# Kernel optimization log

Hardware: AMD Instinct MI355X
Metric: run time of the kernel (lower is better)

## Reference

```python
import jax, jax.numpy as jnp
import numpy as np

H = 512

def setup_inputs() -> dict:
    key = jax.random.key(0)
    ks = jax.random.split(key, 8)
    s = 1.0 / np.sqrt(H)
    return {
        "encoder_outputs": jax.random.normal(ks[0], (64, 2048, H), dtype=jnp.float32),
        "decoder_hidden": jax.random.normal(ks[1], (64, H), dtype=jnp.float32),
        "W1": jax.random.uniform(ks[2], (H, H), jnp.float32, -s, s),
        "b1": jax.random.uniform(ks[3], (H,), jnp.float32, -s, s),
        "W2": jax.random.uniform(ks[4], (H, H), jnp.float32, -s, s),
        "b2": jax.random.uniform(ks[5], (H,), jnp.float32, -s, s),
        "V": jax.random.uniform(ks[6], (H,), jnp.float32, -s, s),  # V weight (1, H) squeezed
        "bv": jax.random.uniform(ks[7], (1,), jnp.float32, -s, s),
    }

def reference(encoder_outputs, decoder_hidden, W1, b1, W2, b2, V, bv):
    # proj of encoder outputs: [B,S,H]; proj of decoder hidden: [B,1,H]
    enc_proj = jnp.einsum('bsh,oh->bso', encoder_outputs, W1) + b1
    dec_proj = (jnp.einsum('bh,oh->bo', decoder_hidden, W2) + b2)[:, None, :]
    energy = jnp.tanh(enc_proj + dec_proj)                      # [B,S,H]
    scores = jnp.einsum('bsh,h->bs', energy, V) + bv[0]          # [B,S]
    attn = jax.nn.softmax(scores, axis=1)                        # [B,S]
    context = jnp.einsum('bs,bsh->bh', attn, encoder_outputs)    # [B,H]
    return context, attn
```

## Files before the change

kernel.cpp:

```cpp
#include <hip/hip_runtime.h>
#include <hip/hip_bf16.h>

typedef __attribute__((ext_vector_type(4))) float f32x4;
typedef __attribute__((ext_vector_type(8))) short s16x8;
typedef __attribute__((ext_vector_type(4))) unsigned short u16x4;
typedef __attribute__((ext_vector_type(8))) __bf16 bf16x8;

#define HDIM 512
#define SEQ  2048
#define NB   64
#define BM   64
#define NBLK ((NB * SEQ) / BM)
#define CPB  (SEQ / BM)

static __device__ __forceinline__ unsigned short f2bf(float f) {
  unsigned u = __float_as_uint(f);
  u += 0x7fffu + ((u >> 16) & 1u);
  return (unsigned short)(u >> 16);
}
static __device__ __forceinline__ float bf2f(unsigned short v) {
  return __uint_as_float(((unsigned)v) << 16);
}

static __device__ __forceinline__ f32x4 mfma16(s16x8 a, s16x8 b, f32x4 c) {
  return __builtin_amdgcn_mfma_f32_16x16x32_bf16(
      __builtin_bit_cast(bf16x8, a), __builtin_bit_cast(bf16x8, b), c, 0, 0, 0);
}

#define BLOADG(dst, sp)                                                        \
  do {                                                                         \
    asm volatile("global_load_dwordx4 %0, %1, %2 offset:0"                     \
                 : "=&v"((dst)[0]) : "v"(voff), "s"(sp));                      \
    asm volatile("global_load_dwordx4 %0, %1, %2 offset:1024"                  \
                 : "=&v"((dst)[1]) : "v"(voff), "s"(sp));                      \
    asm volatile("global_load_dwordx4 %0, %1, %2 offset:2048"                  \
                 : "=&v"((dst)[2]) : "v"(voff), "s"(sp));                      \
    asm volatile("global_load_dwordx4 %0, %1, %2 offset:3072"                  \
                 : "=&v"((dst)[3]) : "v"(voff), "s"(sp));                      \
  } while (0)

#define SLOAD(dst, s)                                                          \
  asm volatile("global_load_dwordx4 %0, %1, %2"                                \
               : "=&v"(dst) : "v"(aoff), "s"(encblk + (s) * 32))

#define WAITV(N)                                                               \
  do {                                                                         \
    asm volatile("s_waitcnt vmcnt(%0)" :: "i"(N) : "memory");                  \
    __builtin_amdgcn_sched_barrier(0);                                         \
  } while (0)

#define PACKW(src, s)                                                          \
  do {                                                                         \
    u16x4 pk;                                                                  \
    pk.x = f2bf((src).x); pk.y = f2bf((src).y);                                \
    pk.z = f2bf((src).z); pk.w = f2bf((src).w);                                \
    *(u16x4*)((char*)Asm + wrow * 1024 +                                       \
              (((((s) * 4) + (wc >> 1)) ^ wr7) * 16) + (wc & 1) * 8) = pk;     \
  } while (0)

__global__ void prep(const float* __restrict__ w1, unsigned short* __restrict__ o,
                     const float* __restrict__ dec, const float* __restrict__ W2,
                     const float* __restrict__ b1, const float* __restrict__ b2,
                     float* __restrict__ zfull) {
  const int bx = blockIdx.x, tid = threadIdx.x;
  if (bx < 128) {
    int id = bx * 256 + tid;
    int kk = id >> 11, n = (id >> 2) & 511, r4 = id & 3;
    const float* src = w1 + (long)n * HDIM + kk * 32 + r4 * 8;
    f32x4 v0 = *(const f32x4*)src;
    f32x4 v1 = *(const f32x4*)(src + 4);
    u16x4 a, b;
    a.x = f2bf(v0.x); a.y = f2bf(v0.y); a.z = f2bf(v0.z); a.w = f2bf(v0.w);
    b.x = f2bf(v1.x); b.y = f2bf(v1.y); b.z = f2bf(v1.z); b.w = f2bf(v1.w);
    unsigned short* dst = o + (long)id * 8;
    *(u16x4*)dst = a;
    *(u16x4*)(dst + 4) = b;
  } else {
    const int idx = bx - 128;
    const int b = idx >> 1, oc = idx & 1;
    const int oo = oc * 256 + tid;
    __shared__ float d_s[HDIM];
    d_s[tid] = dec[b * HDIM + tid];
    d_s[tid + 256] = dec[b * HDIM + tid + 256];
    __syncthreads();
    const float* w = W2 + (long)oo * HDIM;
    float s = 0.f;
#pragma unroll 4
    for (int k = 0; k < HDIM; k += 4) {
      f32x4 v = *(const f32x4*)(w + k);
      s += v.x * d_s[k] + v.y * d_s[k + 1] + v.z * d_s[k + 2] + v.w * d_s[k + 3];
    }
    zfull[b * HDIM + oo] = s + b1[oo] + b2[oo];
  }
}

__global__ __launch_bounds__(512, 4)
void gemm_fused(const float* __restrict__ enc, const unsigned short* __restrict__ w1k,
                const float* __restrict__ zfull, const float* __restrict__ V,
                const float* __restrict__ bv, float* __restrict__ scores,
                unsigned short* __restrict__ pctx, float* __restrict__ ml) {
  __shared__ __align__(16) char pool[67840];
  unsigned short* Asm = (unsigned short*)pool;
  float* red  = (float*)(pool + 65536);
  float* plds = (float*)(pool + 67584);
  float* pcr  = (float*)pool;

  const int tid = threadIdx.x;
  const int wid = tid >> 6;
  const int lane = tid & 63;
  const long m0 = (long)blockIdx.x * BM;
  const int b = (int)(m0 >> 11);

  const int r4 = lane >> 4, c15 = lane & 15, c7 = c15 & 7;
  const char* Ab = (const char*)Asm;
  const unsigned voff = (unsigned)((wid * 64 + c15) * 64 + r4 * 16);
  const int widu = __builtin_amdgcn_readfirstlane(wid);

  const int wrow = tid >> 3, wc = tid & 7, wr7 = wrow & 7;
  const float* encblk = enc + m0 * HDIM;
  const unsigned aoff = (unsigned)(wrow * 2048 + wc * 16);

  {
    f32x4 pa, pb, pc, pd, pe, pf, pg, ph;
    SLOAD(pa, 0); SLOAD(pb, 1); SLOAD(pc, 2); SLOAD(pd, 3);
    SLOAD(pe, 4); SLOAD(pf, 5); SLOAD(pg, 6); SLOAD(ph, 7);
    WAITV(4);
    PACKW(pa, 0); PACKW(pb, 1); PACKW(pc, 2); PACKW(pd, 3);
    SLOAD(pa, 8); SLOAD(pb, 9); SLOAD(pc, 10); SLOAD(pd, 11);
    WAITV(4);
    PACKW(pe, 4); PACKW(pf, 5); PACKW(pg, 6); PACKW(ph, 7);
    SLOAD(pe, 12); SLOAD(pf, 13); SLOAD(pg, 14); SLOAD(ph, 15);
    WAITV(4);
    PACKW(pa, 8); PACKW(pb, 9); PACKW(pc, 10); PACKW(pd, 11);
    WAITV(0);
    PACKW(pe, 12); PACKW(pf, 13); PACKW(pg, 14); PACKW(ph, 15);
  }
  __syncthreads();

  f32x4 acc[4][4] = {};
  s16x8 bX[4], bY[4];

  BLOADG(bX, w1k + ((widu & 15) * 16384));

#pragma unroll
  for (int kk = 0; kk < 16; ++kk) {
    const int ke = (kk + widu) & 15;
    s16x8* cur = (kk & 1) ? bY : bX;
    s16x8* nxt = (kk & 1) ? bX : bY;

    s16x8 af[4];
    const int abase = c15 * 1024 + (((ke * 4 + r4) ^ c7) * 16);
#pragma unroll
    for (int mf = 0; mf < 4; ++mf)
      af[mf] = *(const s16x8*)(Ab + abase + mf * 16384);

    if (kk < 15)
      BLOADG(nxt, w1k + ((((kk + 1) + widu) & 15) * 16384));

    __builtin_amdgcn_s_setprio(1);
    if (kk < 15) {
      WAITV(7);
#pragma unroll
      for (int mf = 0; mf < 4; ++mf) acc[mf][0] = mfma16(af[mf], cur[0], acc[mf][0]);
      WAITV(6);
#pragma unroll
      for (int mf = 0; mf < 4; ++mf) acc[mf][1] = mfma16(af[mf], cur[1], acc[mf][1]);
      WAITV(5);
#pragma unroll
      for (int mf = 0; mf < 4; ++mf) acc[mf][2] = mfma16(af[mf], cur[2], acc[mf][2]);
      WAITV(4);
#pragma unroll
      for (int mf = 0; mf < 4; ++mf) acc[mf][3] = mfma16(af[mf], cur[3], acc[mf][3]);
    } else {
      WAITV(3);
#pragma unroll
      for (int mf = 0; mf < 4; ++mf) acc[mf][0] = mfma16(af[mf], cur[0], acc[mf][0]);
      WAITV(2);
#pragma unroll
      for (int mf = 0; mf < 4; ++mf) acc[mf][1] = mfma16(af[mf], cur[1], acc[mf][1]);
      WAITV(1);
#pragma unroll
      for (int mf = 0; mf < 4; ++mf) acc[mf][2] = mfma16(af[mf], cur[2], acc[mf][2]);
      WAITV(0);
#pragma unroll
      for (int mf = 0; mf < 4; ++mf) acc[mf][3] = mfma16(af[mf], cur[3], acc[mf][3]);
    }
    __builtin_amdgcn_s_setprio(0);
  }

  float zr[4], vr[4];
#pragma unroll
  for (int nf = 0; nf < 4; ++nf) {
    const int n = wid * 64 + nf * 16 + c15;
    zr[nf] = zfull[b * HDIM + n];
    vr[nf] = V[n];
  }
#pragma unroll
  for (int mf = 0; mf < 4; ++mf) {
#pragma unroll
    for (int j = 0; j < 4; ++j) {
      float s = 0.f;
#pragma unroll
      for (int nf = 0; nf < 4; ++nf) {
        float x = acc[mf][nf][j] + zr[nf];
        float e = __expf(2.f * x);
        float t = 1.f - 2.f * __builtin_amdgcn_rcpf(e + 1.f);
        s += t * vr[nf];
      }
      s += __shfl_xor(s, 1); s += __shfl_xor(s, 2);
      s += __shfl_xor(s, 4); s += __shfl_xor(s, 8);
      if (c15 == 0) red[wid * BM + mf * 16 + r4 * 4 + j] = s;
    }
  }
  __syncthreads();

  if (tid < BM) {
    float s = 0.f;
#pragma unroll
    for (int w = 0; w < 8; ++w) s += red[w * BM + tid];
    s += bv[0];
    scores[m0 + tid] = s;
    float mc = s;
#pragma unroll
    for (int off = 1; off < 64; off <<= 1) mc = fmaxf(mc, __shfl_xor(mc, off));
    float p = __expf(s - mc);
    plds[tid] = p;
    float lc = p;
#pragma unroll
    for (int off = 1; off < 64; off <<= 1) lc += __shfl_xor(lc, off);
    if (tid == 0) { ml[blockIdx.x * 2] = mc; ml[blockIdx.x * 2 + 1] = lc; }
  }
  __syncthreads();

  float c8[8] = {};
#pragma unroll
  for (int rr = 0; rr < 8; ++rr) {
    const int r = wid * 8 + rr;
    s16x8 v = *(const s16x8*)(Ab + r * 1024 + ((lane ^ rr) * 16));
    const float p = plds[r];
#pragma unroll
    for (int e = 0; e < 8; ++e)
      c8[e] += p * bf2f((unsigned short)v[e]);
  }
  __syncthreads();
  {
    f32x4 w0, w1;
    w0.x = c8[0]; w0.y = c8[1]; w0.z = c8[2]; w0.w = c8[3];
    w1.x = c8[4]; w1.y = c8[5]; w1.z = c8[6]; w1.w = c8[7];
    *(f32x4*)((char*)pcr + wid * 2048 + lane * 32) = w0;
    *(f32x4*)((char*)pcr + wid * 2048 + lane * 32 + 16) = w1;
  }
  __syncthreads();
  {
    float s = 0.f;
#pragma unroll
    for (int g = 0; g < 8; ++g) s += pcr[g * 512 + tid];
    pctx[(long)blockIdx.x * HDIM + tid] = f2bf(s);
  }
}

__global__ void combine(float* __restrict__ attn, const unsigned short* __restrict__ pctx,
                        const float* __restrict__ ml, float* __restrict__ ctx) {
  const int b = blockIdx.x, tid = threadIdx.x;
  const int lane = tid & 63;
  float m = -1e30f, l = 0.f;
  if (lane < CPB) {
    m = ml[(b * CPB + lane) * 2];
    l = ml[(b * CPB + lane) * 2 + 1];
  }
  float M = m;
#pragma unroll
  for (int off = 1; off < 64; off <<= 1) M = fmaxf(M, __shfl_xor(M, off));
  float le = (lane < CPB) ? l * __expf(m - M) : 0.f;
  float L = le;
#pragma unroll
  for (int off = 1; off < 64; off <<= 1) L += __shfl_xor(L, off);
  const float invL = 1.f / L;

  __shared__ float wc[CPB];
  if (tid < CPB) wc[tid] = __expf(ml[(b * CPB + tid) * 2] - M) * invL;

  float sv[4];
#pragma unroll
  for (int i = 0; i < 4; ++i) sv[i] = attn[(long)b * SEQ + i * 512 + tid];
#pragma unroll
  for (int i = 0; i < 4; ++i)
    attn[(long)b * SEQ + i * 512 + tid] = __expf(sv[i] - M) * invL;

  __syncthreads();
  float a = 0.f;
#pragma unroll 8
  for (int c = 0; c < CPB; ++c)
    a += bf2f(pctx[(long)(b * CPB + c) * HDIM + tid]) * wc[c];
  ctx[(long)b * HDIM + tid] = a;
}

extern "C" void kernel_launch(void* const* d_in, const int* in_sizes, int n_in,
                              void* d_out, int out_size, void* d_ws, size_t ws_size,
                              hipStream_t stream) {
  const float* enc = (const float*)d_in[0];
  const float* dec = (const float*)d_in[1];
  const float* W1  = (const float*)d_in[2];
  const float* b1  = (const float*)d_in[3];
  const float* W2  = (const float*)d_in[4];
  const float* b2  = (const float*)d_in[5];
  const float* V   = (const float*)d_in[6];
  const float* bv  = (const float*)d_in[7];

  float* out  = (float*)d_out;
  float* ctx  = out;
  float* attn = out + NB * HDIM;

  char* ws = (char*)d_ws;
  unsigned short* w1k  = (unsigned short*)ws;
  float*          zful = (float*)(ws + 524288);
  unsigned short* pctx = (unsigned short*)(ws + 655360);
  float*          mlb  = (float*)(ws + 2752512);
  (void)in_sizes; (void)n_in; (void)out_size; (void)ws_size;

  prep<<<256, 256, 0, stream>>>(W1, w1k, dec, W2, b1, b2, zful);
  gemm_fused<<<NBLK, 512, 0, stream>>>(enc, w1k, zful, V, bv, attn, pctx, mlb);
  combine<<<NB, 512, 0, stream>>>(attn, pctx, mlb, ctx);
}
```

Before: 118.1 us.

## Double GEMM row tile to 128 rows per block to reuse W1 fragments

Raises the row tile from 64 to 128 sequence positions per block. Each wave now runs 8 M-fragments against every loaded W1 slice, halving W1 global reads per output row, and LDS grows to about 135KB. The softmax partial reduction becomes a cross-wave reduction through LDS, and occupancy drops from 4 to 2 blocks per CU. The larger accumulator array raises register pressure, and the smaller grid may leave CUs less busy.

```diff
diff --git a/kernel.cpp b/kernel.cpp
--- a/kernel.cpp
+++ b/kernel.cpp
@@ -9,7 +9,7 @@
 #define HDIM 512
 #define SEQ  2048
 #define NB   64
-#define BM   64
+#define BM   128
 #define NBLK ((NB * SEQ) / BM)
 #define CPB  (SEQ / BM)
 
@@ -42,6 +42,9 @@
 #define SLOAD(dst, s)                                                          \
   asm volatile("global_load_dwordx4 %0, %1, %2"                                \
                : "=&v"(dst) : "v"(aoff), "s"(encblk + (s) * 32))
+#define SLOAD2(dst, s)                                                         \
+  asm volatile("global_load_dwordx4 %0, %1, %2"                                \
+               : "=&v"(dst) : "v"(aoff), "s"(encblk + 32768 + (s) * 32))
 
 #define WAITV(N)                                                               \
   do {                                                                         \
@@ -49,12 +52,12 @@
     __builtin_amdgcn_sched_barrier(0);                                         \
   } while (0)
 
-#define PACKW(src, s)                                                          \
+#define PACKWR(src, s, rv)                                                     \
   do {                                                                         \
     u16x4 pk;                                                                  \
     pk.x = f2bf((src).x); pk.y = f2bf((src).y);                                \
     pk.z = f2bf((src).z); pk.w = f2bf((src).w);                                \
-    *(u16x4*)((char*)Asm + wrow * 1024 +                                       \
+    *(u16x4*)((char*)Asm + (rv) * 1024 +                                       \
               (((((s) * 4) + (wc >> 1)) ^ wr7) * 16) + (wc & 1) * 8) = pk;     \
   } while (0)
 
@@ -94,15 +97,17 @@
   }
 }
 
-__global__ __launch_bounds__(512, 4)
+__global__ __launch_bounds__(512, 2)
 void gemm_fused(const float* __restrict__ enc, const unsigned short* __restrict__ w1k,
                 const float* __restrict__ zfull, const float* __restrict__ V,
                 const float* __restrict__ bv, float* __restrict__ scores,
                 unsigned short* __restrict__ pctx, float* __restrict__ ml) {
-  __shared__ __align__(16) char pool[67840];
+  __shared__ __align__(16) char pool[135744];
   unsigned short* Asm = (unsigned short*)pool;
-  float* red  = (float*)(pool + 65536);
-  float* plds = (float*)(pool + 67584);
+  float* red  = (float*)(pool + 131072);
+  float* plds = (float*)(pool + 135168);
+  float* mred = (float*)(pool + 135680);
+  float* lred = (float*)(pool + 135712);
   float* pcr  = (float*)pool;
 
   const int tid = threadIdx.x;
@@ -121,23 +126,40 @@
   const unsigned aoff = (unsigned)(wrow * 2048 + wc * 16);
 
   {
-    f32x4 pa, pb, pc, pd, pe, pf, pg, ph;
-    SLOAD(pa, 0); SLOAD(pb, 1); SLOAD(pc, 2); SLOAD(pd, 3);
-    SLOAD(pe, 4); SLOAD(pf, 5); SLOAD(pg, 6); SLOAD(ph, 7);
-    WAITV(4);
-    PACKW(pa, 0); PACKW(pb, 1); PACKW(pc, 2); PACKW(pd, 3);
-    SLOAD(pa, 8); SLOAD(pb, 9); SLOAD(pc, 10); SLOAD(pd, 11);
-    WAITV(4);
-    PACKW(pe, 4); PACKW(pf, 5); PACKW(pg, 6); PACKW(ph, 7);
-    SLOAD(pe, 12); SLOAD(pf, 13); SLOAD(pg, 14); SLOAD(ph, 15);
-    WAITV(4);
-    PACKW(pa, 8); PACKW(pb, 9); PACKW(pc, 10); PACKW(pd, 11);
+    f32x4 p0, p1, p2, p3, p4, p5, p6, p7;
+    f32x4 q0, q1, q2, q3, q4, q5, q6, q7;
+    SLOAD(p0, 0); SLOAD2(p1, 0); SLOAD(p2, 1); SLOAD2(p3, 1);
+    SLOAD(p4, 2); SLOAD2(p5, 2); SLOAD(p6, 3); SLOAD2(p7, 3);
+    SLOAD(q0, 4); SLOAD2(q1, 4); SLOAD(q2, 5); SLOAD2(q3, 5);
+    SLOAD(q4, 6); SLOAD2(q5, 6); SLOAD(q6, 7); SLOAD2(q7, 7);
+    WAITV(8);
+    PACKWR(p0, 0, wrow); PACKWR(p1, 0, wrow + 64);
+    PACKWR(p2, 1, wrow); PACKWR(p3, 1, wrow + 64);
+    PACKWR(p4, 2, wrow); PACKWR(p5, 2, wrow + 64);
+    PACKWR(p6, 3, wrow); PACKWR(p7, 3, wrow + 64);
+    SLOAD(p0, 8); SLOAD2(p1, 8); SLOAD(p2, 9); SLOAD2(p3, 9);
+    SLOAD(p4, 10); SLOAD2(p5, 10); SLOAD(p6, 11); SLOAD2(p7, 11);
+    WAITV(8);
+    PACKWR(q0, 4, wrow); PACKWR(q1, 4, wrow + 64);
+    PACKWR(q2, 5, wrow); PACKWR(q3, 5, wrow + 64);
+    PACKWR(q4, 6, wrow); PACKWR(q5, 6, wrow + 64);
+    PACKWR(q6, 7, wrow); PACKWR(q7, 7, wrow + 64);
+    SLOAD(q0, 12); SLOAD2(q1, 12); SLOAD(q2, 13); SLOAD2(q3, 13);
+    SLOAD(q4, 14); SLOAD2(q5, 14); SLOAD(q6, 15); SLOAD2(q7, 15);
+    WAITV(8);
+    PACKWR(p0, 8, wrow); PACKWR(p1, 8, wrow + 64);
+    PACKWR(p2, 9, wrow); PACKWR(p3, 9, wrow + 64);
+    PACKWR(p4, 10, wrow); PACKWR(p5, 10, wrow + 64);
+    PACKWR(p6, 11, wrow); PACKWR(p7, 11, wrow + 64);
     WAITV(0);
-    PACKW(pe, 12); PACKW(pf, 13); PACKW(pg, 14); PACKW(ph, 15);
-  }
-  __syncthreads();
-
-  f32x4 acc[4][4] = {};
+    PACKWR(q0, 12, wrow); PACKWR(q1, 12, wrow + 64);
+    PACKWR(q2, 13, wrow); PACKWR(q3, 13, wrow + 64);
+    PACKWR(q4, 14, wrow); PACKWR(q5, 14, wrow + 64);
+    PACKWR(q6, 15, wrow); PACKWR(q7, 15, wrow + 64);
+  }
+  __syncthreads();
+
+  f32x4 acc[8][4] = {};
   s16x8 bX[4], bY[4];
 
   BLOADG(bX, w1k + ((widu & 15) * 16384));
@@ -148,10 +170,10 @@
     s16x8* cur = (kk & 1) ? bY : bX;
     s16x8* nxt = (kk & 1) ? bX : bY;
 
-    s16x8 af[4];
+    s16x8 af[8];
     const int abase = c15 * 1024 + (((ke * 4 + r4) ^ c7) * 16);
 #pragma unroll
-    for (int mf = 0; mf < 4; ++mf)
+    for (int mf = 0; mf < 8; ++mf)
       af[mf] = *(const s16x8*)(Ab + abase + mf * 16384);
 
     if (kk < 15)
@@ -161,29 +183,29 @@
     if (kk < 15) {
       WAITV(7);
 #pragma unroll
-      for (int mf = 0; mf < 4; ++mf) acc[mf][0] = mfma16(af[mf], cur[0], acc[mf][0]);
+      for (int mf = 0; mf < 8; ++mf) acc[mf][0] = mfma16(af[mf], cur[0], acc[mf][0]);
       WAITV(6);
 #pragma unroll
-      for (int mf = 0; mf < 4; ++mf) acc[mf][1] = mfma16(af[mf], cur[1], acc[mf][1]);
+      for (int mf = 0; mf < 8; ++mf) acc[mf][1] = mfma16(af[mf], cur[1], acc[mf][1]);
       WAITV(5);
 #pragma unroll
-      for (int mf = 0; mf < 4; ++mf) acc[mf][2] = mfma16(af[mf], cur[2], acc[mf][2]);
+      for (int mf = 0; mf < 8; ++mf) acc[mf][2] = mfma16(af[mf], cur[2], acc[mf][2]);
       WAITV(4);
 #pragma unroll
-      for (int mf = 0; mf < 4; ++mf) acc[mf][3] = mfma16(af[mf], cur[3], acc[mf][3]);
+      for (int mf = 0; mf < 8; ++mf) acc[mf][3] = mfma16(af[mf], cur[3], acc[mf][3]);
     } else {
       WAITV(3);
 #pragma unroll
-      for (int mf = 0; mf < 4; ++mf) acc[mf][0] = mfma16(af[mf], cur[0], acc[mf][0]);
+      for (int mf = 0; mf < 8; ++mf) acc[mf][0] = mfma16(af[mf], cur[0], acc[mf][0]);
       WAITV(2);
 #pragma unroll
-      for (int mf = 0; mf < 4; ++mf) acc[mf][1] = mfma16(af[mf], cur[1], acc[mf][1]);
+      for (int mf = 0; mf < 8; ++mf) acc[mf][1] = mfma16(af[mf], cur[1], acc[mf][1]);
       WAITV(1);
 #pragma unroll
-      for (int mf = 0; mf < 4; ++mf) acc[mf][2] = mfma16(af[mf], cur[2], acc[mf][2]);
+      for (int mf = 0; mf < 8; ++mf) acc[mf][2] = mfma16(af[mf], cur[2], acc[mf][2]);
       WAITV(0);
 #pragma unroll
-      for (int mf = 0; mf < 4; ++mf) acc[mf][3] = mfma16(af[mf], cur[3], acc[mf][3]);
+      for (int mf = 0; mf < 8; ++mf) acc[mf][3] = mfma16(af[mf], cur[3], acc[mf][3]);
     }
     __builtin_amdgcn_s_setprio(0);
   }
@@ -196,7 +218,7 @@
     vr[nf] = V[n];
   }
 #pragma unroll
-  for (int mf = 0; mf < 4; ++mf) {
+  for (int mf = 0; mf < 8; ++mf) {
 #pragma unroll
     for (int j = 0; j < 4; ++j) {
       float s = 0.f;
@@ -214,29 +236,41 @@
   }
   __syncthreads();
 
+  float sv = 0.f, pv = 0.f;
   if (tid < BM) {
     float s = 0.f;
 #pragma unroll
     for (int w = 0; w < 8; ++w) s += red[w * BM + tid];
     s += bv[0];
     scores[m0 + tid] = s;
-    float mc = s;
-#pragma unroll
-    for (int off = 1; off < 64; off <<= 1) mc = fmaxf(mc, __shfl_xor(mc, off));
-    float p = __expf(s - mc);
-    plds[tid] = p;
-    float lc = p;
-#pragma unroll
-    for (int off = 1; off < 64; off <<= 1) lc += __shfl_xor(lc, off);
-    if (tid == 0) { ml[blockIdx.x * 2] = mc; ml[blockIdx.x * 2 + 1] = lc; }
-  }
-  __syncthreads();
+    sv = s;
+  }
+  float mc = (tid < BM) ? sv : -1e30f;
+#pragma unroll
+  for (int off = 1; off < 64; off <<= 1) mc = fmaxf(mc, __shfl_xor(mc, off));
+  if (lane == 0) mred[wid] = mc;
+  __syncthreads();
+  float M = mred[0];
+#pragma unroll
+  for (int w = 1; w < 8; ++w) M = fmaxf(M, mred[w]);
+  if (tid < BM) { pv = __expf(sv - M); plds[tid] = pv; }
+  float lc = pv;
+#pragma unroll
+  for (int off = 1; off < 64; off <<= 1) lc += __shfl_xor(lc, off);
+  if (lane == 0) lred[wid] = lc;
+  __syncthreads();
+  if (tid == 0) {
+    float L = 0.f;
+#pragma unroll
+    for (int w = 0; w < 8; ++w) L += lred[w];
+    ml[blockIdx.x * 2] = M; ml[blockIdx.x * 2 + 1] = L;
+  }
 
   float c8[8] = {};
 #pragma unroll
-  for (int rr = 0; rr < 8; ++rr) {
-    const int r = wid * 8 + rr;
-    s16x8 v = *(const s16x8*)(Ab + r * 1024 + ((lane ^ rr) * 16));
+  for (int rr = 0; rr < 16; ++rr) {
+    const int r = wid * 16 + rr;
+    s16x8 v = *(const s16x8*)(Ab + r * 1024 + ((lane ^ (rr & 7)) * 16));
     const float p = plds[r];
 #pragma unroll
     for (int e = 0; e < 8; ++e)
```

New measurement: 138.2 us. 1.17x slower.

## Double row tile to 128 with 1024-thread blocks and triple-buffered W1 loads

Applied to the files above, without the earlier changes.

Doubles the encoder rows handled per block to 128 and uses 16 waves, each covering 32 output columns over 8 M-fragments. This raises reuse of each streamed W1 fragment and halves the number of partial-context and max/sum records that combine has to merge. W1 fragments are now triple-buffered with a single wait per k-step, and the per-wave staggered k order is dropped. The block softmax statistics become a cross-wave reduction through LDS. The cost is about 137 KB of LDS per block, which limits each CU to one resident block and reduces latency hiding.

```diff
diff --git a/kernel.cpp b/kernel.cpp
--- a/kernel.cpp
+++ b/kernel.cpp
@@ -9,7 +9,7 @@
 #define HDIM 512
 #define SEQ  2048
 #define NB   64
-#define BM   64
+#define BM   128
 #define NBLK ((NB * SEQ) / BM)
 #define CPB  (SEQ / BM)
 
@@ -27,16 +27,12 @@
       __builtin_bit_cast(bf16x8, a), __builtin_bit_cast(bf16x8, b), c, 0, 0, 0);
 }
 
-#define BLOADG(dst, sp)                                                        \
+#define BLOADG2(dst, sp)                                                       \
   do {                                                                         \
     asm volatile("global_load_dwordx4 %0, %1, %2 offset:0"                     \
                  : "=&v"((dst)[0]) : "v"(voff), "s"(sp));                      \
     asm volatile("global_load_dwordx4 %0, %1, %2 offset:1024"                  \
                  : "=&v"((dst)[1]) : "v"(voff), "s"(sp));                      \
-    asm volatile("global_load_dwordx4 %0, %1, %2 offset:2048"                  \
-                 : "=&v"((dst)[2]) : "v"(voff), "s"(sp));                      \
-    asm volatile("global_load_dwordx4 %0, %1, %2 offset:3072"                  \
-                 : "=&v"((dst)[3]) : "v"(voff), "s"(sp));                      \
   } while (0)
 
 #define SLOAD(dst, s)                                                          \
@@ -94,15 +90,17 @@
   }
 }
 
-__global__ __launch_bounds__(512, 4)
+__global__ __launch_bounds__(1024, 4)
 void gemm_fused(const float* __restrict__ enc, const unsigned short* __restrict__ w1k,
                 const float* __restrict__ zfull, const float* __restrict__ V,
                 const float* __restrict__ bv, float* __restrict__ scores,
                 unsigned short* __restrict__ pctx, float* __restrict__ ml) {
-  __shared__ __align__(16) char pool[67840];
+  __shared__ __align__(16) char pool[139904];
   unsigned short* Asm = (unsigned short*)pool;
-  float* red  = (float*)(pool + 65536);
-  float* plds = (float*)(pool + 67584);
+  float* red  = (float*)(pool + 131072);
+  float* plds = (float*)(pool + 139264);
+  float* mred = (float*)(pool + 139776);
+  float* lred = (float*)(pool + 139840);
   float* pcr  = (float*)pool;
 
   const int tid = threadIdx.x;
@@ -113,8 +111,7 @@
 
   const int r4 = lane >> 4, c15 = lane & 15, c7 = c15 & 7;
   const char* Ab = (const char*)Asm;
-  const unsigned voff = (unsigned)((wid * 64 + c15) * 64 + r4 * 16);
-  const int widu = __builtin_amdgcn_readfirstlane(wid);
+  const unsigned voff = (unsigned)((wid * 32 + c15) * 64 + r4 * 16);
 
   const int wrow = tid >> 3, wc = tid & 7, wr7 = wrow & 7;
   const float* encblk = enc + m0 * HDIM;
@@ -137,71 +134,47 @@
   }
   __syncthreads();
 
-  f32x4 acc[4][4] = {};
-  s16x8 bX[4], bY[4];
-
-  BLOADG(bX, w1k + ((widu & 15) * 16384));
+  f32x4 acc[8][2] = {};
+  s16x8 bq[3][2];
+
+  BLOADG2(bq[0], w1k);
+  BLOADG2(bq[1], w1k + 16384);
 
 #pragma unroll
   for (int kk = 0; kk < 16; ++kk) {
-    const int ke = (kk + widu) & 15;
-    s16x8* cur = (kk & 1) ? bY : bX;
-    s16x8* nxt = (kk & 1) ? bX : bY;
-
-    s16x8 af[4];
-    const int abase = c15 * 1024 + (((ke * 4 + r4) ^ c7) * 16);
-#pragma unroll
-    for (int mf = 0; mf < 4; ++mf)
-      af[mf] = *(const s16x8*)(Ab + abase + mf * 16384);
-
-    if (kk < 15)
-      BLOADG(nxt, w1k + ((((kk + 1) + widu) & 15) * 16384));
-
+    if (kk < 14)
+      BLOADG2(bq[(kk + 2) % 3], w1k + (kk + 2) * 16384);
+
+    if (kk < 14)      WAITV(4);
+    else if (kk == 14) WAITV(2);
+    else               WAITV(0);
+
+    const int abase = c15 * 1024 + (((kk * 4 + r4) ^ c7) * 16);
+    const s16x8* cur = bq[kk % 3];
     __builtin_amdgcn_s_setprio(1);
-    if (kk < 15) {
-      WAITV(7);
-#pragma unroll
-      for (int mf = 0; mf < 4; ++mf) acc[mf][0] = mfma16(af[mf], cur[0], acc[mf][0]);
-      WAITV(6);
-#pragma unroll
-      for (int mf = 0; mf < 4; ++mf) acc[mf][1] = mfma16(af[mf], cur[1], acc[mf][1]);
-      WAITV(5);
-#pragma unroll
-      for (int mf = 0; mf < 4; ++mf) acc[mf][2] = mfma16(af[mf], cur[2], acc[mf][2]);
-      WAITV(4);
-#pragma unroll
-      for (int mf = 0; mf < 4; ++mf) acc[mf][3] = mfma16(af[mf], cur[3], acc[mf][3]);
-    } else {
-      WAITV(3);
-#pragma unroll
-      for (int mf = 0; mf < 4; ++mf) acc[mf][0] = mfma16(af[mf], cur[0], acc[mf][0]);
-      WAITV(2);
-#pragma unroll
-      for (int mf = 0; mf < 4; ++mf) acc[mf][1] = mfma16(af[mf], cur[1], acc[mf][1]);
-      WAITV(1);
-#pragma unroll
-      for (int mf = 0; mf < 4; ++mf) acc[mf][2] = mfma16(af[mf], cur[2], acc[mf][2]);
-      WAITV(0);
-#pragma unroll
-      for (int mf = 0; mf < 4; ++mf) acc[mf][3] = mfma16(af[mf], cur[3], acc[mf][3]);
+#pragma unroll
+    for (int mf = 0; mf < 8; ++mf) {
+      s16x8 af = *(const s16x8*)(Ab + abase + mf * 16384);
+      acc[mf][0] = mfma16(af, cur[0], acc[mf][0]);
+      acc[mf][1] = mfma16(af, cur[1], acc[mf][1]);
     }
     __builtin_amdgcn_s_setprio(0);
   }
 
-  float zr[4], vr[4];
-#pragma unroll
-  for (int nf = 0; nf < 4; ++nf) {
-    const int n = wid * 64 + nf * 16 + c15;
+  float zr[2], vr[2];
+#pragma unroll
+  for (int nf = 0; nf < 2; ++nf) {
+    const int n = wid * 32 + nf * 16 + c15;
     zr[nf] = zfull[b * HDIM + n];
     vr[nf] = V[n];
   }
 #pragma unroll
-  for (int mf = 0; mf < 4; ++mf) {
+  for (int mf = 0; mf < 8; ++mf) {
 #pragma unroll
     for (int j = 0; j < 4; ++j) {
       float s = 0.f;
 #pragma unroll
-      for (int nf = 0; nf < 4; ++nf) {
+      for (int nf = 0; nf < 2; ++nf) {
         float x = acc[mf][nf][j] + zr[nf];
         float e = __expf(2.f * x);
         float t = 1.f - 2.f * __builtin_amdgcn_rcpf(e + 1.f);
@@ -214,29 +187,41 @@
   }
   __syncthreads();
 
+  float sv = -1e30f, pv = 0.f;
   if (tid < BM) {
     float s = 0.f;
 #pragma unroll
-    for (int w = 0; w < 8; ++w) s += red[w * BM + tid];
+    for (int w = 0; w < 16; ++w) s += red[w * BM + tid];
     s += bv[0];
     scores[m0 + tid] = s;
-    float mc = s;
-#pragma unroll
-    for (int off = 1; off < 64; off <<= 1) mc = fmaxf(mc, __shfl_xor(mc, off));
-    float p = __expf(s - mc);
-    plds[tid] = p;
-    float lc = p;
-#pragma unroll
-    for (int off = 1; off < 64; off <<= 1) lc += __shfl_xor(lc, off);
-    if (tid == 0) { ml[blockIdx.x * 2] = mc; ml[blockIdx.x * 2 + 1] = lc; }
-  }
-  __syncthreads();
+    sv = s;
+  }
+  float mc = sv;
+#pragma unroll
+  for (int off = 1; off < 64; off <<= 1) mc = fmaxf(mc, __shfl_xor(mc, off));
+  if (lane == 0) mred[wid] = mc;
+  __syncthreads();
+  float M = mred[0];
+#pragma unroll
+  for (int w = 1; w < 16; ++w) M = fmaxf(M, mred[w]);
+  if (tid < BM) { pv = __expf(sv - M); plds[tid] = pv; }
+  float lc = pv;
+#pragma unroll
+  for (int off = 1; off < 64; off <<= 1) lc += __shfl_xor(lc, off);
+  if (lane == 0) lred[wid] = lc;
+  __syncthreads();
+  if (tid == 0) {
+    float L = 0.f;
+#pragma unroll
+    for (int w = 0; w < 16; ++w) L += lred[w];
+    ml[blockIdx.x * 2] = M; ml[blockIdx.x * 2 + 1] = L;
+  }
 
   float c8[8] = {};
 #pragma unroll
   for (int rr = 0; rr < 8; ++rr) {
     const int r = wid * 8 + rr;
-    s16x8 v = *(const s16x8*)(Ab + r * 1024 + ((lane ^ rr) * 16));
+    s16x8 v = *(const s16x8*)(Ab + r * 1024 + ((lane ^ (r & 7)) * 16));
     const float p = plds[r];
 #pragma unroll
     for (int e = 0; e < 8; ++e)
@@ -251,10 +236,10 @@
     *(f32x4*)((char*)pcr + wid * 2048 + lane * 32 + 16) = w1;
   }
   __syncthreads();
-  {
+  if (tid < HDIM) {
     float s = 0.f;
 #pragma unroll
-    for (int g = 0; g < 8; ++g) s += pcr[g * 512 + tid];
+    for (int g = 0; g < 16; ++g) s += pcr[g * 512 + tid];
     pctx[(long)blockIdx.x * HDIM + tid] = f2bf(s);
   }
 }
@@ -319,6 +304,6 @@
   (void)in_sizes; (void)n_in; (void)out_size; (void)ws_size;
 
   prep<<<256, 256, 0, stream>>>(W1, w1k, dec, W2, b1, b2, zful);
-  gemm_fused<<<NBLK, 512, 0, stream>>>(enc, w1k, zful, V, bv, attn, pctx, mlb);
+  gemm_fused<<<NBLK, 1024, 0, stream>>>(enc, w1k, zful, V, bv, attn, pctx, mlb);
   combine<<<NB, 512, 0, stream>>>(attn, pctx, mlb, ctx);
 }
```

Measured after the change: 141.5 us. 1.2x slower.
